# Kernel tuning notes

Hardware: AMD Instinct MI355X
Metric: run time of the kernel (lower is better)

## Reference

```python
import jax, jax.numpy as jnp
import numpy as np

B, IN, H, T = 64, 16, 512, 1024


def setup_inputs() -> dict:
    key = jax.random.key(0)
    ks = jax.random.split(key, 14)
    s = 0.05  # small init scale for numerically stable recurrence
    inp = {
        "x": jax.random.normal(ks[0], (B, IN), dtype=jnp.float32),
        "w_in": jax.random.normal(ks[1], (H, IN), dtype=jnp.float32) * s,
        "b_in": jax.random.normal(ks[2], (H,), dtype=jnp.float32) * s,
        "w_ih0": jax.random.normal(ks[3], (4 * H, H), dtype=jnp.float32) * s,
        "w_hh0": jax.random.normal(ks[4], (4 * H, H), dtype=jnp.float32) * s,
        "b_ih0": jax.random.normal(ks[5], (4 * H,), dtype=jnp.float32) * s,
        "b_hh0": jax.random.normal(ks[6], (4 * H,), dtype=jnp.float32) * s,
        "w_ih1": jax.random.normal(ks[7], (4 * H, H), dtype=jnp.float32) * s,
        "w_hh1": jax.random.normal(ks[8], (4 * H, H), dtype=jnp.float32) * s,
        "b_ih1": jax.random.normal(ks[9], (4 * H,), dtype=jnp.float32) * s,
        "b_hh1": jax.random.normal(ks[10], (4 * H,), dtype=jnp.float32) * s,
        "w_out": jax.random.normal(ks[11], (1, H), dtype=jnp.float32) * s,
        "b_out": jax.random.normal(ks[12], (1,), dtype=jnp.float32) * s,
        "seq_len": T,
    }
    return inp


def _lstm_layer(x_seq, w_ih, w_hh, b_ih, b_hh):
    # x_seq: [T, B, H] time-major. PyTorch gate order: i, f, g, o.
    # Precompute input-to-hidden projection for all steps at once.
    xg = jnp.einsum('tbh,gh->tbg', x_seq, w_ih) + b_ih  # [T, B, 4H]
    Bn = x_seq.shape[1]
    Hn = w_hh.shape[1]

    def step(carry, xg_t):
        h, c = carry
        g = xg_t + h @ w_hh.T + b_hh  # [B, 4H]
        i, f, gg, o = jnp.split(g, 4, axis=-1)
        c = jax.nn.sigmoid(f) * c + jax.nn.sigmoid(i) * jnp.tanh(gg)
        h = jax.nn.sigmoid(o) * jnp.tanh(c)
        return (h, c), h

    init = (jnp.zeros((Bn, Hn), x_seq.dtype), jnp.zeros((Bn, Hn), x_seq.dtype))
    _, hs = jax.lax.scan(step, init, xg)
    return hs  # [T, B, H]


def reference(x, w_in, b_in, w_ih0, w_hh0, b_ih0, b_hh0,
              w_ih1, w_hh1, b_ih1, b_hh1, w_out, b_out, seq_len):
    # fc_in then broadcast the identical input across all timesteps
    h_in = x @ w_in.T + b_in                      # [B, H]
    x_seq = jnp.broadcast_to(h_in[None], (seq_len, h_in.shape[0], h_in.shape[1]))
    h = _lstm_layer(x_seq, w_ih0, w_hh0, b_ih0, b_hh0)
    h = _lstm_layer(h, w_ih1, w_hh1, b_ih1, b_hh1)
    out = h @ w_out.T + b_out                     # [T, B, 1]
    return jnp.transpose(out, (1, 0, 2))          # [B, T, 1] (batch_first)
```

## Files before the change

kernel.cpp:

```cpp
#include <hip/hip_runtime.h>
#include <stdint.h>


#define TSEQ 1024
#define HDIM 512
#define BATCH 64
#define RING 8

typedef __attribute__((ext_vector_type(8))) short bf16x8;
typedef __attribute__((ext_vector_type(4))) float f32x4;
typedef __attribute__((ext_vector_type(4))) unsigned int u32x4;

__device__ __forceinline__ unsigned short f2bf(float f) {
  union { float f; unsigned u; } v; v.f = f;
  unsigned r = v.u + 0x7FFFu + ((v.u >> 16) & 1u);
  return (unsigned short)(r >> 16);
}
__device__ __forceinline__ float bf2f(unsigned short s) {
  union { unsigned u; float f; } v; v.u = ((unsigned)s) << 16; return v.f;
}
__device__ __forceinline__ float sigm(float x) { return 1.0f / (1.0f + __expf(-x)); }
__device__ __forceinline__ float tanh_(float x) { return 1.0f - 2.0f / (__expf(2.0f * x) + 1.0f); }

__device__ __forceinline__ void flag_add(int* p) {
  __hip_atomic_fetch_add(p, 1, __ATOMIC_RELAXED, __HIP_MEMORY_SCOPE_AGENT);
}
__device__ __forceinline__ void flag_wait(int* p, int target) {
  while (__hip_atomic_load(p, __ATOMIC_RELAXED, __HIP_MEMORY_SCOPE_AGENT) < target)
    __builtin_amdgcn_s_sleep(1);
}

__device__ __forceinline__ void stage64k(char* lds, const unsigned short* src, int tid) {
  u32x4 r0, r1, r2, r3, r4, r5, r6, r7;
  const char* a = (const char*)src + (size_t)tid * 16;
  asm volatile(
      "global_load_dwordx4 %0, %8, off sc1\n\t"
      "global_load_dwordx4 %1, %9, off sc1\n\t"
      "global_load_dwordx4 %2, %10, off sc1\n\t"
      "global_load_dwordx4 %3, %11, off sc1\n\t"
      "global_load_dwordx4 %4, %12, off sc1\n\t"
      "global_load_dwordx4 %5, %13, off sc1\n\t"
      "global_load_dwordx4 %6, %14, off sc1\n\t"
      "global_load_dwordx4 %7, %15, off sc1\n\t"
      "s_waitcnt vmcnt(0)"
      : "=&v"(r0), "=&v"(r1), "=&v"(r2), "=&v"(r3),
        "=&v"(r4), "=&v"(r5), "=&v"(r6), "=&v"(r7)
      : "v"(a), "v"(a + 8192), "v"(a + 16384), "v"(a + 24576),
        "v"(a + 32768), "v"(a + 40960), "v"(a + 49152), "v"(a + 57344)
      : "memory");
  u32x4 vv[8] = {r0, r1, r2, r3, r4, r5, r6, r7};
  #pragma unroll
  for (int i = 0; i < 8; ++i) {
    int q = tid + i * 512;
    int row = q >> 6, kb = (q & 63) << 4;
    *(u32x4*)(lds + row * 1024 + (kb ^ ((row & 7) << 4))) = vv[i];
  }
}
__device__ __forceinline__ void zero64k(char* lds, int tid) {
  u32x4 z = {0u, 0u, 0u, 0u};
  #pragma unroll
  for (int i = 0; i < 8; ++i) {
    int q = tid + i * 512;
    int row = q >> 6, kb = (q & 63) << 4;
    *(u32x4*)(lds + row * 1024 + (kb ^ ((row & 7) << 4))) = z;
  }
}

__global__ void k_fc_in(const float* __restrict__ x, const float* __restrict__ w_in,
                        const float* __restrict__ b_in, float* __restrict__ h_in) {
  int b = blockIdx.x;
  int j = threadIdx.x;
  float acc = b_in[j];
  #pragma unroll
  for (int i = 0; i < 16; ++i) acc += x[b * 16 + i] * w_in[j * 16 + i];
  h_in[b * HDIM + j] = acc;
}

__global__ __launch_bounds__(512, 1)
void k_xg0(const float* __restrict__ h_in, const float* __restrict__ w_ih0,
           const float* __restrict__ b_ih0, const float* __restrict__ b_hh0,
           float* __restrict__ xg0) {
  __shared__ float hbuf[64 * 516];
  __shared__ float wbuf[8 * 520];
  int r0 = blockIdx.x * 8;
  int tid = threadIdx.x;
  for (int i = 0; i < 64; ++i) {
    int c = tid + i * 512;
    hbuf[(c >> 9) * 516 + (c & 511)] = h_in[c];
  }
  for (int i = 0; i < 8; ++i) {
    int c = tid + i * 512;
    wbuf[(c >> 9) * 520 + (c & 511)] = w_ih0[(size_t)r0 * HDIM + c];
  }
  __syncthreads();
  int b = tid >> 3, rl = tid & 7;
  float acc = 0.f;
  for (int k = 0; k < 512; ++k) acc += hbuf[b * 516 + k] * wbuf[rl * 520 + k];
  int r = r0 + rl;
  xg0[(size_t)b * 2048 + r] = acc + b_ih0[r] + b_hh0[r];
}

__global__ __launch_bounds__(512, 1)
void lstm_persist(const float* __restrict__ w_hh0,
                  const float* __restrict__ w_ih1,
                  const float* __restrict__ w_hh1,
                  const float* __restrict__ b_ih1,
                  const float* __restrict__ b_hh1,
                  const float* __restrict__ w_out,
                  const float* __restrict__ b_out,
                  const float* __restrict__ xg0,
                  unsigned short* __restrict__ h0_ring,
                  unsigned short* __restrict__ h1_ring,
                  int* __restrict__ flags,
                  float* __restrict__ out) {
  __shared__ __align__(16) unsigned short hA[BATCH * HDIM];
  __shared__ __align__(16) unsigned short hBt[BATCH * HDIM];
  __shared__ float gbuf[BATCH * 68];
  char* hAc = (char*)hA;
  char* hBc = (char*)hBt;

  const int tid = threadIdx.x;
  const int layer = blockIdx.x & 1;
  const int p = blockIdx.x >> 1;
  const int u0 = p * 16;

  const int wave = tid >> 6, lane = tid & 63;
  const int nt = wave & 3;
  const int mh = wave >> 2;
  const int ln15 = lane & 15, lg = lane >> 4;

  const int n_local = nt * 16 + ln15;
  const int grow = (n_local & 3) * HDIM + u0 + (n_local >> 2);

  int* h0_ready = flags;
  int* h0_done  = flags + TSEQ;
  int* h1_ready = flags + 2 * TSEQ;
  int* h1_done  = flags + 3 * TSEQ;

  bf16x8 wh[16];
  bf16x8 wi[16];
  {
    const float* Wh = (layer == 0 ? w_hh0 : w_hh1) + (size_t)grow * HDIM;
    #pragma unroll
    for (int kt = 0; kt < 16; ++kt) {
      const float* s = Wh + kt * 32 + lg * 8;
      bf16x8 r;
      #pragma unroll
      for (int e = 0; e < 8; ++e) r[e] = (short)f2bf(s[e]);
      wh[kt] = r;
    }
  }
  if (layer == 1) {
    const float* Wi = w_ih1 + (size_t)grow * HDIM;
    #pragma unroll
    for (int kt = 0; kt < 16; ++kt) {
      const float* s = Wi + kt * 32 + lg * 8;
      bf16x8 r;
      #pragma unroll
      for (int e = 0; e < 8; ++e) r[e] = (short)f2bf(s[e]);
      wi[kt] = r;
    }
  }

  f32x4 init0, init1;
  if (layer == 0) {
    #pragma unroll
    for (int r = 0; r < 4; ++r) {
      init0[r] = xg0[(size_t)(mh * 32 + lg * 4 + r) * 2048 + grow];
      init1[r] = xg0[(size_t)(mh * 32 + 16 + lg * 4 + r) * 2048 + grow];
    }
  } else {
    float bv = b_ih1[grow] + b_hh1[grow];
    #pragma unroll
    for (int r = 0; r < 4; ++r) { init0[r] = bv; init1[r] = bv; }
  }

  float c0 = 0.f, c1 = 0.f;
  const int pb = tid >> 3;
  const int pu = (tid << 1) & 15;

  const int r0 = mh * 32 + ln15, r1 = r0 + 16;
  const int x0 = (r0 & 7) << 4, x1 = (r1 & 7) << 4;

  if (layer == 0) {
    for (int t = 0; t < TSEQ; ++t) {
      if (t > 0) {
        if (tid == 0) flag_wait(&h0_ready[t - 1], 32);
        __syncthreads();
        stage64k(hAc, h0_ring + (size_t)((t - 1) & (RING - 1)) * (BATCH * HDIM), tid);
        __syncthreads();
        if (tid == 0) flag_add(&h0_done[t - 1]);
      } else {
        zero64k(hAc, tid);
        __syncthreads();
      }
      f32x4 a0 = init0, a1 = init1;
      #pragma unroll
      for (int kt = 0; kt < 16; ++kt) {
        const int kb = kt * 64 + lg * 16;
        bf16x8 ha0 = *(const bf16x8*)(hAc + r0 * 1024 + (kb ^ x0));
        bf16x8 ha1 = *(const bf16x8*)(hAc + r1 * 1024 + (kb ^ x1));
        a0 = __builtin_amdgcn_mfma_f32_16x16x32_bf16(ha0, wh[kt], a0, 0, 0, 0);
        a1 = __builtin_amdgcn_mfma_f32_16x16x32_bf16(ha1, wh[kt], a1, 0, 0, 0);
      }
      #pragma unroll
      for (int r = 0; r < 4; ++r) {
        gbuf[(mh * 32 + lg * 4 + r) * 68 + n_local] = a0[r];
        gbuf[(mh * 32 + 16 + lg * 4 + r) * 68 + n_local] = a1[r];
      }
      if (t >= RING && tid == 0) flag_wait(&h0_done[t - RING], 64);
      __syncthreads();
      {
        f32x4 gA = *(const f32x4*)&gbuf[pb * 68 + pu * 4];
        f32x4 gB = *(const f32x4*)&gbuf[pb * 68 + pu * 4 + 4];
        float i0 = sigm(gA[0]), f0 = sigm(gA[1]), z0 = tanh_(gA[2]), o0 = sigm(gA[3]);
        float i1 = sigm(gB[0]), f1 = sigm(gB[1]), z1 = tanh_(gB[2]), o1 = sigm(gB[3]);
        c0 = f0 * c0 + i0 * z0;
        c1 = f1 * c1 + i1 * z1;
        float hv0 = o0 * tanh_(c0), hv1 = o1 * tanh_(c1);
        unsigned pk = (unsigned)f2bf(hv0) | ((unsigned)f2bf(hv1) << 16);
        unsigned short* slot = h0_ring + (size_t)(t & (RING - 1)) * (BATCH * HDIM);
        __hip_atomic_store((unsigned*)(slot + pb * HDIM + u0 + pu), pk,
                           __ATOMIC_RELAXED, __HIP_MEMORY_SCOPE_AGENT);
      }
      __syncthreads();
      if (tid == 0) flag_add(&h0_ready[t]);
    }
  } else {
    for (int t = 0; t < TSEQ; ++t) {
      if (tid == 0) {
        flag_wait(&h0_ready[t], 32);
        if (t > 0) flag_wait(&h1_ready[t - 1], 32);
      }
      __syncthreads();
      stage64k(hAc, h0_ring + (size_t)(t & (RING - 1)) * (BATCH * HDIM), tid);
      if (t > 0)
        stage64k(hBc, h1_ring + (size_t)((t - 1) & (RING - 1)) * (BATCH * HDIM), tid);
      else
        zero64k(hBc, tid);
      __syncthreads();
      if (tid == 0) {
        flag_add(&h0_done[t]);
        if (t > 0) flag_add(&h1_done[t - 1]);
      }

      if (t > 0 && tid < 16) {
        const int b = 2 * p + (tid >> 3), seg = tid & 7;
        const int xb = (b & 7) << 4;
        float acc = 0.f;
        #pragma unroll
        for (int i = 0; i < 8; ++i) {
          const int kb = seg * 128 + i * 16;
          bf16x8 hv = *(const bf16x8*)(hBc + b * 1024 + (kb ^ xb));
          const float* wo = w_out + (kb >> 1);
          #pragma unroll
          for (int e = 0; e < 8; ++e) acc += bf2f((unsigned short)hv[e]) * wo[e];
        }
        acc += __shfl_down(acc, 4, 8);
        acc += __shfl_down(acc, 2, 8);
        acc += __shfl_down(acc, 1, 8);
        if (seg == 0) out[b * TSEQ + (t - 1)] = acc + b_out[0];
      }

      f32x4 a0 = init0, a1 = init1;
      #pragma unroll
      for (int kt = 0; kt < 16; ++kt) {
        const int kb = kt * 64 + lg * 16;
        bf16x8 ia0 = *(const bf16x8*)(hAc + r0 * 1024 + (kb ^ x0));
        bf16x8 ia1 = *(const bf16x8*)(hAc + r1 * 1024 + (kb ^ x1));
        bf16x8 ha0 = *(const bf16x8*)(hBc + r0 * 1024 + (kb ^ x0));
        bf16x8 ha1 = *(const bf16x8*)(hBc + r1 * 1024 + (kb ^ x1));
        a0 = __builtin_amdgcn_mfma_f32_16x16x32_bf16(ia0, wi[kt], a0, 0, 0, 0);
        a1 = __builtin_amdgcn_mfma_f32_16x16x32_bf16(ia1, wi[kt], a1, 0, 0, 0);
        a0 = __builtin_amdgcn_mfma_f32_16x16x32_bf16(ha0, wh[kt], a0, 0, 0, 0);
        a1 = __builtin_amdgcn_mfma_f32_16x16x32_bf16(ha1, wh[kt], a1, 0, 0, 0);
      }
      #pragma unroll
      for (int r = 0; r < 4; ++r) {
        gbuf[(mh * 32 + lg * 4 + r) * 68 + n_local] = a0[r];
        gbuf[(mh * 32 + 16 + lg * 4 + r) * 68 + n_local] = a1[r];
      }
      if (t >= RING && tid == 0) flag_wait(&h1_done[t - RING], 32);
      __syncthreads();
      {
        f32x4 gA = *(const f32x4*)&gbuf[pb * 68 + pu * 4];
        f32x4 gB = *(const f32x4*)&gbuf[pb * 68 + pu * 4 + 4];
        float i0 = sigm(gA[0]), f0 = sigm(gA[1]), z0 = tanh_(gA[2]), o0 = sigm(gA[3]);
        float i1 = sigm(gB[0]), f1 = sigm(gB[1]), z1 = tanh_(gB[2]), o1 = sigm(gB[3]);
        c0 = f0 * c0 + i0 * z0;
        c1 = f1 * c1 + i1 * z1;
        float hv0 = o0 * tanh_(c0), hv1 = o1 * tanh_(c1);
        unsigned pk = (unsigned)f2bf(hv0) | ((unsigned)f2bf(hv1) << 16);
        unsigned short* slot = h1_ring + (size_t)(t & (RING - 1)) * (BATCH * HDIM);
        __hip_atomic_store((unsigned*)(slot + pb * HDIM + u0 + pu), pk,
                           __ATOMIC_RELAXED, __HIP_MEMORY_SCOPE_AGENT);
      }
      __syncthreads();
      if (tid == 0) flag_add(&h1_ready[t]);
    }
    if (tid == 0) flag_wait(&h1_ready[TSEQ - 1], 32);
    __syncthreads();
    stage64k(hBc, h1_ring + (size_t)((TSEQ - 1) & (RING - 1)) * (BATCH * HDIM), tid);
    __syncthreads();
    if (tid < 16) {
      const int b = 2 * p + (tid >> 3), seg = tid & 7;
      const int xb = (b & 7) << 4;
      float acc = 0.f;
      #pragma unroll
      for (int i = 0; i < 8; ++i) {
        const int kb = seg * 128 + i * 16;
        bf16x8 hv = *(const bf16x8*)(hBc + b * 1024 + (kb ^ xb));
        const float* wo = w_out + (kb >> 1);
        #pragma unroll
        for (int e = 0; e < 8; ++e) acc += bf2f((unsigned short)hv[e]) * wo[e];
      }
      acc += __shfl_down(acc, 4, 8);
      acc += __shfl_down(acc, 2, 8);
      acc += __shfl_down(acc, 1, 8);
      if (seg == 0) out[b * TSEQ + (TSEQ - 1)] = acc + b_out[0];
    }
  }
}

extern "C" void kernel_launch(void* const* d_in, const int* in_sizes, int n_in,
                              void* d_out, int out_size, void* d_ws, size_t ws_size,
                              hipStream_t stream) {
  (void)in_sizes; (void)n_in; (void)out_size; (void)ws_size;
  const float* x     = (const float*)d_in[0];
  const float* w_in  = (const float*)d_in[1];
  const float* b_in  = (const float*)d_in[2];
  const float* w_ih0 = (const float*)d_in[3];
  const float* w_hh0 = (const float*)d_in[4];
  const float* b_ih0 = (const float*)d_in[5];
  const float* b_hh0 = (const float*)d_in[6];
  const float* w_ih1 = (const float*)d_in[7];
  const float* w_hh1 = (const float*)d_in[8];
  const float* b_ih1 = (const float*)d_in[9];
  const float* b_hh1 = (const float*)d_in[10];
  const float* w_out = (const float*)d_in[11];
  const float* b_out = (const float*)d_in[12];

  char* ws = (char*)d_ws;
  unsigned short* h0_ring = (unsigned short*)(ws + 0);
  unsigned short* h1_ring = (unsigned short*)(ws + 524288);
  float* xg0  = (float*)(ws + 1048576);
  float* h_in = (float*)(ws + 1572864);
  int*   flags = (int*)(ws + 1703936);

  hipMemsetAsync(flags, 0, 4 * TSEQ * sizeof(int), stream);
  k_fc_in<<<64, 512, 0, stream>>>(x, w_in, b_in, h_in);
  k_xg0<<<256, 512, 0, stream>>>(h_in, w_ih0, b_ih0, b_hh0, xg0);
  lstm_persist<<<64, 512, 0, stream>>>(w_hh0, w_ih1, w_hh1, b_ih1, b_hh1,
                                       w_out, b_out, xg0, h0_ring, h1_ring,
                                       flags, (float*)d_out);
}
```

Measured before the change: 5.963 ms.

## Replace shared ready counters with per-producer sequence flags and packed publish

```diff
diff --git a/kernel.cpp b/kernel.cpp
--- a/kernel.cpp
+++ b/kernel.cpp
@@ -10,6 +10,7 @@
 typedef __attribute__((ext_vector_type(8))) short bf16x8;
 typedef __attribute__((ext_vector_type(4))) float f32x4;
 typedef __attribute__((ext_vector_type(4))) unsigned int u32x4;
+typedef unsigned long long u64;
 
 __device__ __forceinline__ unsigned short f2bf(float f) {
   union { float f; unsigned u; } v; v.f = f;
@@ -22,12 +23,24 @@
 __device__ __forceinline__ float sigm(float x) { return 1.0f / (1.0f + __expf(-x)); }
 __device__ __forceinline__ float tanh_(float x) { return 1.0f - 2.0f / (__expf(2.0f * x) + 1.0f); }
 
+__device__ __forceinline__ int g_ld32(const int* p) {
+  return __hip_atomic_load(p, __ATOMIC_RELAXED, __HIP_MEMORY_SCOPE_AGENT);
+}
+__device__ __forceinline__ void g_st32(int* p, int v) {
+  __hip_atomic_store(p, v, __ATOMIC_RELAXED, __HIP_MEMORY_SCOPE_AGENT);
+}
+__device__ __forceinline__ void g_st64(u64* p, u64 v) {
+  __hip_atomic_store(p, v, __ATOMIC_RELAXED, __HIP_MEMORY_SCOPE_AGENT);
+}
 __device__ __forceinline__ void flag_add(int* p) {
   __hip_atomic_fetch_add(p, 1, __ATOMIC_RELAXED, __HIP_MEMORY_SCOPE_AGENT);
 }
 __device__ __forceinline__ void flag_wait(int* p, int target) {
-  while (__hip_atomic_load(p, __ATOMIC_RELAXED, __HIP_MEMORY_SCOPE_AGENT) < target)
-    __builtin_amdgcn_s_sleep(1);
+  while (g_ld32(p) < target) __builtin_amdgcn_s_sleep(1);
+}
+__device__ __forceinline__ void poll_seq(const int* f, int tgt, int lane) {
+  const int* a = f + (lane & 31) * 4;
+  while (!__all(g_ld32(a) >= tgt)) __builtin_amdgcn_s_sleep(1);
 }
 
 __device__ __forceinline__ void stage64k(char* lds, const unsigned short* src, int tid) {
@@ -52,18 +65,26 @@
   #pragma unroll
   for (int i = 0; i < 8; ++i) {
     int q = tid + i * 512;
-    int row = q >> 6, kb = (q & 63) << 4;
-    *(u32x4*)(lds + row * 1024 + (kb ^ ((row & 7) << 4))) = vv[i];
+    int b = (q >> 1) & 63;
+    int col = (((q >> 7) << 5) | ((q & 1) << 4)) ^ ((b & 7) << 4);
+    *(u32x4*)(lds + b * 1024 + col) = vv[i];
   }
 }
 __device__ __forceinline__ void zero64k(char* lds, int tid) {
   u32x4 z = {0u, 0u, 0u, 0u};
   #pragma unroll
-  for (int i = 0; i < 8; ++i) {
-    int q = tid + i * 512;
-    int row = q >> 6, kb = (q & 63) << 4;
-    *(u32x4*)(lds + row * 1024 + (kb ^ ((row & 7) << 4))) = z;
-  }
+  for (int i = 0; i < 8; ++i)
+    *(u32x4*)(lds + (size_t)(tid + i * 512) * 16) = z;
+}
+
+__device__ __forceinline__ void publish2k(char* slotbase, int p, const unsigned short* hpk,
+                                          int lane, int* flagword, int val) {
+  const u64* s = (const u64*)(hpk + lane * 16);
+  u64 v0 = s[0], v1 = s[1], v2 = s[2], v3 = s[3];
+  u64* d = (u64*)(slotbase + p * 2048 + lane * 32);
+  g_st64(d + 0, v0); g_st64(d + 1, v1); g_st64(d + 2, v2); g_st64(d + 3, v3);
+  asm volatile("s_waitcnt vmcnt(0)" ::: "memory");
+  if (lane == 0) g_st32(flagword, val);
 }
 
 __global__ void k_fc_in(const float* __restrict__ x, const float* __restrict__ w_in,
@@ -109,13 +130,15 @@
                   const float* __restrict__ w_out,
                   const float* __restrict__ b_out,
                   const float* __restrict__ xg0,
-                  unsigned short* __restrict__ h0_ring,
-                  unsigned short* __restrict__ h1_ring,
+                  unsigned short* __restrict__ ring0,
+                  unsigned short* __restrict__ ring1,
                   int* __restrict__ flags,
                   float* __restrict__ out) {
   __shared__ __align__(16) unsigned short hA[BATCH * HDIM];
   __shared__ __align__(16) unsigned short hBt[BATCH * HDIM];
   __shared__ float gbuf[BATCH * 68];
+  __shared__ __align__(16) unsigned short hpk[BATCH * 16];
+  __shared__ float wout_s[HDIM];
   char* hAc = (char*)hA;
   char* hBc = (char*)hBt;
 
@@ -132,10 +155,13 @@
   const int n_local = nt * 16 + ln15;
   const int grow = (n_local & 3) * HDIM + u0 + (n_local >> 2);
 
-  int* h0_ready = flags;
-  int* h0_done  = flags + TSEQ;
-  int* h1_ready = flags + 2 * TSEQ;
-  int* h1_done  = flags + 3 * TSEQ;
+  int* f0 = flags;
+  int* f1 = flags + 128;
+  int* h0_done = flags + 256;
+  int* h1_done = flags + 256 + TSEQ;
+
+  wout_s[tid] = w_out[tid];
+  const float bout = b_out[0];
 
   bf16x8 wh[16];
   bf16x8 wi[16];
@@ -182,18 +208,19 @@
   const int r0 = mh * 32 + ln15, r1 = r0 + 16;
   const int x0 = (r0 & 7) << 4, x1 = (r1 & 7) << 4;
 
+  const int ob = tid >> 2, oseg = tid & 3;
+  const int oxs = (ob & 7) << 4;
+
   if (layer == 0) {
     for (int t = 0; t < TSEQ; ++t) {
-      if (t > 0) {
-        if (tid == 0) flag_wait(&h0_ready[t - 1], 32);
-        __syncthreads();
-        stage64k(hAc, h0_ring + (size_t)((t - 1) & (RING - 1)) * (BATCH * HDIM), tid);
-        __syncthreads();
-        if (tid == 0) flag_add(&h0_done[t - 1]);
-      } else {
-        zero64k(hAc, tid);
-        __syncthreads();
-      }
+      if (wave == 0) { if (t > 0) poll_seq(f0, t, lane); }
+      else if (wave == 1 && lane == 0 && t >= RING) flag_wait(&h0_done[t - RING], 64);
+      __syncthreads();
+      if (t > 0) stage64k(hAc, ring0 + (size_t)((t - 1) & (RING - 1)) * (BATCH * HDIM), tid);
+      else       zero64k(hAc, tid);
+      __syncthreads();
+      if (tid == 0 && t > 0) flag_add(&h0_done[t - 1]);
+
       f32x4 a0 = init0, a1 = init1;
       #pragma unroll
       for (int kt = 0; kt < 16; ++kt) {
@@ -208,58 +235,50 @@
         gbuf[(mh * 32 + lg * 4 + r) * 68 + n_local] = a0[r];
         gbuf[(mh * 32 + 16 + lg * 4 + r) * 68 + n_local] = a1[r];
       }
-      if (t >= RING && tid == 0) flag_wait(&h0_done[t - RING], 64);
       __syncthreads();
       {
         f32x4 gA = *(const f32x4*)&gbuf[pb * 68 + pu * 4];
         f32x4 gB = *(const f32x4*)&gbuf[pb * 68 + pu * 4 + 4];
-        float i0 = sigm(gA[0]), f0 = sigm(gA[1]), z0 = tanh_(gA[2]), o0 = sigm(gA[3]);
-        float i1 = sigm(gB[0]), f1 = sigm(gB[1]), z1 = tanh_(gB[2]), o1 = sigm(gB[3]);
-        c0 = f0 * c0 + i0 * z0;
-        c1 = f1 * c1 + i1 * z1;
-        float hv0 = o0 * tanh_(c0), hv1 = o1 * tanh_(c1);
-        unsigned pk = (unsigned)f2bf(hv0) | ((unsigned)f2bf(hv1) << 16);
-        unsigned short* slot = h0_ring + (size_t)(t & (RING - 1)) * (BATCH * HDIM);
-        __hip_atomic_store((unsigned*)(slot + pb * HDIM + u0 + pu), pk,
-                           __ATOMIC_RELAXED, __HIP_MEMORY_SCOPE_AGENT);
-      }
-      __syncthreads();
-      if (tid == 0) flag_add(&h0_ready[t]);
+        float i0 = sigm(gA[0]), f0v = sigm(gA[1]), z0 = tanh_(gA[2]), o0 = sigm(gA[3]);
+        float i1 = sigm(gB[0]), f1v = sigm(gB[1]), z1 = tanh_(gB[2]), o1 = sigm(gB[3]);
+        c0 = f0v * c0 + i0 * z0;
+        c1 = f1v * c1 + i1 * z1;
+        unsigned pk = (unsigned)f2bf(o0 * tanh_(c0)) | ((unsigned)f2bf(o1 * tanh_(c1)) << 16);
+        *(unsigned*)&hpk[pb * 16 + pu] = pk;
+      }
+      __syncthreads();
+      if (wave == 0)
+        publish2k((char*)(ring0 + (size_t)(t & (RING - 1)) * (BATCH * HDIM)),
+                  p, hpk, lane, &f0[p * 4], t + 1);
     }
   } else {
     for (int t = 0; t < TSEQ; ++t) {
-      if (tid == 0) {
-        flag_wait(&h0_ready[t], 32);
-        if (t > 0) flag_wait(&h1_ready[t - 1], 32);
-      }
-      __syncthreads();
-      stage64k(hAc, h0_ring + (size_t)(t & (RING - 1)) * (BATCH * HDIM), tid);
-      if (t > 0)
-        stage64k(hBc, h1_ring + (size_t)((t - 1) & (RING - 1)) * (BATCH * HDIM), tid);
-      else
-        zero64k(hBc, tid);
+      if (wave == 0) poll_seq(f0, t + 1, lane);
+      else if (wave == 1) { if (t > 0) poll_seq(f1, t, lane); }
+      else if (wave == 2 && lane == 0 && t >= RING) flag_wait(&h1_done[t - RING], 32);
+      __syncthreads();
+      stage64k(hAc, ring0 + (size_t)(t & (RING - 1)) * (BATCH * HDIM), tid);
+      if (t > 0) stage64k(hBc, ring1 + (size_t)((t - 1) & (RING - 1)) * (BATCH * HDIM), tid);
+      else       zero64k(hBc, tid);
       __syncthreads();
       if (tid == 0) {
         flag_add(&h0_done[t]);
         if (t > 0) flag_add(&h1_done[t - 1]);
       }
 
-      if (t > 0 && tid < 16) {
-        const int b = 2 * p + (tid >> 3), seg = tid & 7;
-        const int xb = (b & 7) << 4;
-        float acc = 0.f;
+      if (t > 0 && tid < 256) {
+        float od = 0.f;
         #pragma unroll
-        for (int i = 0; i < 8; ++i) {
-          const int kb = seg * 128 + i * 16;
-          bf16x8 hv = *(const bf16x8*)(hBc + b * 1024 + (kb ^ xb));
-          const float* wo = w_out + (kb >> 1);
+        for (int j = 0; j < 16; ++j) {
+          const int c = (j * 4 + oseg) * 16;
+          bf16x8 hv = *(const bf16x8*)(hBc + ob * 1024 + (c ^ oxs));
+          const float* wo = &wout_s[c >> 1];
           #pragma unroll
-          for (int e = 0; e < 8; ++e) acc += bf2f((unsigned short)hv[e]) * wo[e];
+          for (int e = 0; e < 8; ++e) od += bf2f((unsigned short)hv[e]) * wo[e];
         }
-        acc += __shfl_down(acc, 4, 8);
-        acc += __shfl_down(acc, 2, 8);
-        acc += __shfl_down(acc, 1, 8);
-        if (seg == 0) out[b * TSEQ + (t - 1)] = acc + b_out[0];
+        od += __shfl_xor(od, 1);
+        od += __shfl_xor(od, 2);
+        if (oseg == 0) out[ob * TSEQ + (t - 1)] = od + bout;
       }
 
       f32x4 a0 = init0, a1 = init1;
@@ -280,44 +299,39 @@
         gbuf[(mh * 32 + lg * 4 + r) * 68 + n_local] = a0[r];
         gbuf[(mh * 32 + 16 + lg * 4 + r) * 68 + n_local] = a1[r];
       }
-      if (t >= RING && tid == 0) flag_wait(&h1_done[t - RING], 32);
       __syncthreads();
       {
         f32x4 gA = *(const f32x4*)&gbuf[pb * 68 + pu * 4];
         f32x4 gB = *(const f32x4*)&gbuf[pb * 68 + pu * 4 + 4];
-        float i0 = sigm(gA[0]), f0 = sigm(gA[1]), z0 = tanh_(gA[2]), o0 = sigm(gA[3]);
-        float i1 = sigm(gB[0]), f1 = sigm(gB[1]), z1 = tanh_(gB[2]), o1 = sigm(gB[3]);
-        c0 = f0 * c0 + i0 * z0;
-        c1 = f1 * c1 + i1 * z1;
-        float hv0 = o0 * tanh_(c0), hv1 = o1 * tanh_(c1);
-        unsigned pk = (unsigned)f2bf(hv0) | ((unsigned)f2bf(hv1) << 16);
-        unsigned short* slot = h1_ring + (size_t)(t & (RING - 1)) * (BATCH * HDIM);
-        __hip_atomic_store((unsigned*)(slot + pb * HDIM + u0 + pu), pk,
-                           __ATOMIC_RELAXED, __HIP_MEMORY_SCOPE_AGENT);
-      }
-      __syncthreads();
-      if (tid == 0) flag_add(&h1_ready[t]);
-    }
-    if (tid == 0) flag_wait(&h1_ready[TSEQ - 1], 32);
+        float i0 = sigm(gA[0]), f0v = sigm(gA[1]), z0 = tanh_(gA[2]), o0 = sigm(gA[3]);
+        float i1 = sigm(gB[0]), f1v = sigm(gB[1]), z1 = tanh_(gB[2]), o1 = sigm(gB[3]);
+        c0 = f0v * c0 + i0 * z0;
+        c1 = f1v * c1 + i1 * z1;
+        unsigned pk = (unsigned)f2bf(o0 * tanh_(c0)) | ((unsigned)f2bf(o1 * tanh_(c1)) << 16);
+        *(unsigned*)&hpk[pb * 16 + pu] = pk;
+      }
+      __syncthreads();
+      if (wave == 0)
+        publish2k((char*)(ring1 + (size_t)(t & (RING - 1)) * (BATCH * HDIM)),
+                  p, hpk, lane, &f1[p * 4], t + 1);
+    }
+    if (wave == 0) poll_seq(f1, TSEQ, lane);
     __syncthreads();
-    stage64k(hBc, h1_ring + (size_t)((TSEQ - 1) & (RING - 1)) * (BATCH * HDIM), tid);
+    stage64k(hBc, ring1 + (size_t)((TSEQ - 1) & (RING - 1)) * (BATCH * HDIM), tid);
     __syncthreads();
-    if (tid < 16) {
-      const int b = 2 * p + (tid >> 3), seg = tid & 7;
-      const int xb = (b & 7) << 4;
-      float acc = 0.f;
-      #pragma unroll
-      for (int i = 0; i < 8; ++i) {
-        const int kb = seg * 128 + i * 16;
-        bf16x8 hv = *(const bf16x8*)(hBc + b * 1024 + (kb ^ xb));
-        const float* wo = w_out + (kb >> 1);
+    if (tid < 256) {
+      float od = 0.f;
+      #pragma unroll
+      for (int j = 0; j < 16; ++j) {
+        const int c = (j * 4 + oseg) * 16;
+        bf16x8 hv = *(const bf16x8*)(hBc + ob * 1024 + (c ^ oxs));
+        const float* wo = &wout_s[c >> 1];
         #pragma unroll
-        for (int e = 0; e < 8; ++e) acc += bf2f((unsigned short)hv[e]) * wo[e];
-      }
-      acc += __shfl_down(acc, 4, 8);
-      acc += __shfl_down(acc, 2, 8);
-      acc += __shfl_down(acc, 1, 8);
-      if (seg == 0) out[b * TSEQ + (TSEQ - 1)] = acc + b_out[0];
+        for (int e = 0; e < 8; ++e) od += bf2f((unsigned short)hv[e]) * wo[e];
+      }
+      od += __shfl_xor(od, 1);
+      od += __shfl_xor(od, 2);
+      if (oseg == 0) out[ob * TSEQ + (TSEQ - 1)] = od + bout;
     }
   }
 }
@@ -341,16 +355,16 @@
   const float* b_out = (const float*)d_in[12];
 
   char* ws = (char*)d_ws;
-  unsigned short* h0_ring = (unsigned short*)(ws + 0);
-  unsigned short* h1_ring = (unsigned short*)(ws + 524288);
+  unsigned short* ring0 = (unsigned short*)(ws + 0);
+  unsigned short* ring1 = (unsigned short*)(ws + 524288);
   float* xg0  = (float*)(ws + 1048576);
   float* h_in = (float*)(ws + 1572864);
   int*   flags = (int*)(ws + 1703936);
 
-  hipMemsetAsync(flags, 0, 4 * TSEQ * sizeof(int), stream);
+  hipMemsetAsync(flags, 0, 16384, stream);
   k_fc_in<<<64, 512, 0, stream>>>(x, w_in, b_in, h_in);
   k_xg0<<<256, 512, 0, stream>>>(h_in, w_ih0, b_ih0, b_hh0, xg0);
   lstm_persist<<<64, 512, 0, stream>>>(w_hh0, w_ih1, w_hh1, b_ih1, b_hh1,
-                                       w_out, b_out, xg0, h0_ring, h1_ring,
+                                       w_out, b_out, xg0, ring0, ring1,
                                        flags, (float*)d_out);
 }
```

Result: slower. 7.418 ms (+24.4%).

## Replace per-step atomic counter flags with per-block sequence flags polled by a wave

Applied to the files above, without the earlier changes.

```diff
diff --git a/kernel.cpp b/kernel.cpp
--- a/kernel.cpp
+++ b/kernel.cpp
@@ -22,12 +22,27 @@
 __device__ __forceinline__ float sigm(float x) { return 1.0f / (1.0f + __expf(-x)); }
 __device__ __forceinline__ float tanh_(float x) { return 1.0f - 2.0f / (__expf(2.0f * x) + 1.0f); }
 
+__device__ __forceinline__ int g_ld32(const int* p) {
+  return __hip_atomic_load(p, __ATOMIC_RELAXED, __HIP_MEMORY_SCOPE_AGENT);
+}
+__device__ __forceinline__ void g_st32(int* p, int v) {
+  __hip_atomic_store(p, v, __ATOMIC_RELAXED, __HIP_MEMORY_SCOPE_AGENT);
+}
 __device__ __forceinline__ void flag_add(int* p) {
   __hip_atomic_fetch_add(p, 1, __ATOMIC_RELAXED, __HIP_MEMORY_SCOPE_AGENT);
 }
 __device__ __forceinline__ void flag_wait(int* p, int target) {
-  while (__hip_atomic_load(p, __ATOMIC_RELAXED, __HIP_MEMORY_SCOPE_AGENT) < target)
-    __builtin_amdgcn_s_sleep(1);
+  while (g_ld32(p) < target) __builtin_amdgcn_s_sleep(1);
+}
+__device__ __forceinline__ void poll_seq(const int* f, int tgt, int lane) {
+  const int* a = f + (lane & 31) * 4;
+  while (!__all(g_ld32(a) >= tgt)) __builtin_amdgcn_s_sleep(1);
+}
+__device__ __forceinline__ void poll_seq2(const int* fa, int ta,
+                                          const int* fb, int tb, int lane) {
+  const int* a = (lane < 32) ? (fa + lane * 4) : (fb + (lane - 32) * 4);
+  const int tgt = (lane < 32) ? ta : tb;
+  while (!__all(g_ld32(a) >= tgt)) __builtin_amdgcn_s_sleep(1);
 }
 
 __device__ __forceinline__ void stage64k(char* lds, const unsigned short* src, int tid) {
@@ -132,10 +147,10 @@
   const int n_local = nt * 16 + ln15;
   const int grow = (n_local & 3) * HDIM + u0 + (n_local >> 2);
 
-  int* h0_ready = flags;
-  int* h0_done  = flags + TSEQ;
-  int* h1_ready = flags + 2 * TSEQ;
-  int* h1_done  = flags + 3 * TSEQ;
+  int* f0seq = flags;
+  int* f1seq = flags + 128;
+  int* h0_done = flags + 256;
+  int* h1_done = flags + 256 + TSEQ;
 
   bf16x8 wh[16];
   bf16x8 wi[16];
@@ -184,9 +199,9 @@
 
   if (layer == 0) {
     for (int t = 0; t < TSEQ; ++t) {
+      if (t > 0 && wave == 0) poll_seq(f0seq, t, lane);
+      __syncthreads();
       if (t > 0) {
-        if (tid == 0) flag_wait(&h0_ready[t - 1], 32);
-        __syncthreads();
         stage64k(hAc, h0_ring + (size_t)((t - 1) & (RING - 1)) * (BATCH * HDIM), tid);
         __syncthreads();
         if (tid == 0) flag_add(&h0_done[t - 1]);
@@ -224,14 +239,11 @@
                            __ATOMIC_RELAXED, __HIP_MEMORY_SCOPE_AGENT);
       }
       __syncthreads();
-      if (tid == 0) flag_add(&h0_ready[t]);
+      if (tid == 0) g_st32(&f0seq[p * 4], t + 1);
     }
   } else {
     for (int t = 0; t < TSEQ; ++t) {
-      if (tid == 0) {
-        flag_wait(&h0_ready[t], 32);
-        if (t > 0) flag_wait(&h1_ready[t - 1], 32);
-      }
+      if (wave == 0) poll_seq2(f0seq, t + 1, f1seq, t, lane);
       __syncthreads();
       stage64k(hAc, h0_ring + (size_t)(t & (RING - 1)) * (BATCH * HDIM), tid);
       if (t > 0)
@@ -296,9 +308,9 @@
                            __ATOMIC_RELAXED, __HIP_MEMORY_SCOPE_AGENT);
       }
       __syncthreads();
-      if (tid == 0) flag_add(&h1_ready[t]);
-    }
-    if (tid == 0) flag_wait(&h1_ready[TSEQ - 1], 32);
+      if (tid == 0) g_st32(&f1seq[p * 4], t + 1);
+    }
+    if (wave == 0) poll_seq(f1seq, TSEQ, lane);
     __syncthreads();
     stage64k(hBc, h1_ring + (size_t)((TSEQ - 1) & (RING - 1)) * (BATCH * HDIM), tid);
     __syncthreads();
@@ -347,7 +359,7 @@
   float* h_in = (float*)(ws + 1572864);
   int*   flags = (int*)(ws + 1703936);
 
-  hipMemsetAsync(flags, 0, 4 * TSEQ * sizeof(int), stream);
+  hipMemsetAsync(flags, 0, 16384, stream);
   k_fc_in<<<64, 512, 0, stream>>>(x, w_in, b_in, h_in);
   k_xg0<<<256, 512, 0, stream>>>(h_in, w_ih0, b_ih0, b_hh0, xg0);
   lstm_persist<<<64, 512, 0, stream>>>(w_hh0, w_ih1, w_hh1, b_ih1, b_hh1,
```

Measured after the change: 6.333 ms. +6.2%, slower.

## Replace ready-flag handshakes with per-word timestep tags in hidden-state ring

Applied to the files above, without the earlier changes.

```diff
diff --git a/kernel.cpp b/kernel.cpp
--- a/kernel.cpp
+++ b/kernel.cpp
@@ -29,41 +29,63 @@
   while (__hip_atomic_load(p, __ATOMIC_RELAXED, __HIP_MEMORY_SCOPE_AGENT) < target)
     __builtin_amdgcn_s_sleep(1);
 }
-
-__device__ __forceinline__ void stage64k(char* lds, const unsigned short* src, int tid) {
-  u32x4 r0, r1, r2, r3, r4, r5, r6, r7;
-  const char* a = (const char*)src + (size_t)tid * 16;
-  asm volatile(
-      "global_load_dwordx4 %0, %8, off sc1\n\t"
-      "global_load_dwordx4 %1, %9, off sc1\n\t"
-      "global_load_dwordx4 %2, %10, off sc1\n\t"
-      "global_load_dwordx4 %3, %11, off sc1\n\t"
-      "global_load_dwordx4 %4, %12, off sc1\n\t"
-      "global_load_dwordx4 %5, %13, off sc1\n\t"
-      "global_load_dwordx4 %6, %14, off sc1\n\t"
-      "global_load_dwordx4 %7, %15, off sc1\n\t"
-      "s_waitcnt vmcnt(0)"
-      : "=&v"(r0), "=&v"(r1), "=&v"(r2), "=&v"(r3),
-        "=&v"(r4), "=&v"(r5), "=&v"(r6), "=&v"(r7)
-      : "v"(a), "v"(a + 8192), "v"(a + 16384), "v"(a + 24576),
-        "v"(a + 32768), "v"(a + 40960), "v"(a + 49152), "v"(a + 57344)
-      : "memory");
-  u32x4 vv[8] = {r0, r1, r2, r3, r4, r5, r6, r7};
+__device__ __forceinline__ void g_st32u(unsigned* p, unsigned v) {
+  __hip_atomic_store(p, v, __ATOMIC_RELAXED, __HIP_MEMORY_SCOPE_AGENT);
+}
+
+__device__ __forceinline__ void stage_tag(char* lds, const unsigned* src32,
+                                          int tid, int tag) {
   #pragma unroll
-  for (int i = 0; i < 8; ++i) {
-    int q = tid + i * 512;
-    int row = q >> 6, kb = (q & 63) << 4;
-    *(u32x4*)(lds + row * 1024 + (kb ^ ((row & 7) << 4))) = vv[i];
+  for (int half = 0; half < 2; ++half) {
+    u32x4 r0, r1, r2, r3, r4, r5, r6, r7;
+    const char* a = (const char*)src32 + (size_t)tid * 32 + (size_t)half * 65536;
+    while (true) {
+      asm volatile(
+          "global_load_dwordx4 %0, %8, off sc1\n\t"
+          "global_load_dwordx4 %1, %9, off sc1\n\t"
+          "global_load_dwordx4 %2, %10, off sc1\n\t"
+          "global_load_dwordx4 %3, %11, off sc1\n\t"
+          "global_load_dwordx4 %4, %12, off sc1\n\t"
+          "global_load_dwordx4 %5, %13, off sc1\n\t"
+          "global_load_dwordx4 %6, %14, off sc1\n\t"
+          "global_load_dwordx4 %7, %15, off sc1\n\t"
+          "s_waitcnt vmcnt(0)"
+          : "=&v"(r0), "=&v"(r1), "=&v"(r2), "=&v"(r3),
+            "=&v"(r4), "=&v"(r5), "=&v"(r6), "=&v"(r7)
+          : "v"(a), "v"(a + 16), "v"(a + 16384), "v"(a + 16400),
+            "v"(a + 32768), "v"(a + 32784), "v"(a + 49152), "v"(a + 49168)
+          : "memory");
+      bool ok = true;
+      #pragma unroll
+      for (int j = 0; j < 4; ++j) {
+        ok &= ((r0[j] & 0xffffu) == (unsigned)tag) & ((r1[j] & 0xffffu) == (unsigned)tag);
+        ok &= ((r2[j] & 0xffffu) == (unsigned)tag) & ((r3[j] & 0xffffu) == (unsigned)tag);
+        ok &= ((r4[j] & 0xffffu) == (unsigned)tag) & ((r5[j] & 0xffffu) == (unsigned)tag);
+        ok &= ((r6[j] & 0xffffu) == (unsigned)tag) & ((r7[j] & 0xffffu) == (unsigned)tag);
+      }
+      if (__all(ok)) break;
+      __builtin_amdgcn_s_sleep(1);
+    }
+    u32x4 lo[4] = {r0, r2, r4, r6};
+    u32x4 hi[4] = {r1, r3, r5, r7};
+    #pragma unroll
+    for (int j = 0; j < 4; ++j) {
+      int q = tid + (4 * half + j) * 512;
+      int row = q >> 6, kb = (q & 63) << 4;
+      u32x4 outq;
+      outq[0] = (lo[j][1] & 0xffff0000u) | (lo[j][0] >> 16);
+      outq[1] = (lo[j][3] & 0xffff0000u) | (lo[j][2] >> 16);
+      outq[2] = (hi[j][1] & 0xffff0000u) | (hi[j][0] >> 16);
+      outq[3] = (hi[j][3] & 0xffff0000u) | (hi[j][2] >> 16);
+      *(u32x4*)(lds + row * 1024 + (kb ^ ((row & 7) << 4))) = outq;
+    }
   }
 }
 __device__ __forceinline__ void zero64k(char* lds, int tid) {
   u32x4 z = {0u, 0u, 0u, 0u};
   #pragma unroll
-  for (int i = 0; i < 8; ++i) {
-    int q = tid + i * 512;
-    int row = q >> 6, kb = (q & 63) << 4;
-    *(u32x4*)(lds + row * 1024 + (kb ^ ((row & 7) << 4))) = z;
-  }
+  for (int i = 0; i < 8; ++i)
+    *(u32x4*)(lds + (size_t)(tid + i * 512) * 16) = z;
 }
 
 __global__ void k_fc_in(const float* __restrict__ x, const float* __restrict__ w_in,
@@ -109,8 +131,8 @@
                   const float* __restrict__ w_out,
                   const float* __restrict__ b_out,
                   const float* __restrict__ xg0,
-                  unsigned short* __restrict__ h0_ring,
-                  unsigned short* __restrict__ h1_ring,
+                  unsigned* __restrict__ ring0,
+                  unsigned* __restrict__ ring1,
                   int* __restrict__ flags,
                   float* __restrict__ out) {
   __shared__ __align__(16) unsigned short hA[BATCH * HDIM];
@@ -132,10 +154,8 @@
   const int n_local = nt * 16 + ln15;
   const int grow = (n_local & 3) * HDIM + u0 + (n_local >> 2);
 
-  int* h0_ready = flags;
-  int* h0_done  = flags + TSEQ;
-  int* h1_ready = flags + 2 * TSEQ;
-  int* h1_done  = flags + 3 * TSEQ;
+  int* h0_done = flags;
+  int* h1_done = flags + TSEQ;
 
   bf16x8 wh[16];
   bf16x8 wi[16];
@@ -182,18 +202,15 @@
   const int r0 = mh * 32 + ln15, r1 = r0 + 16;
   const int x0 = (r0 & 7) << 4, x1 = (r1 & 7) << 4;
 
+  const size_t SL32 = (size_t)BATCH * HDIM;
+
   if (layer == 0) {
     for (int t = 0; t < TSEQ; ++t) {
-      if (t > 0) {
-        if (tid == 0) flag_wait(&h0_ready[t - 1], 32);
-        __syncthreads();
-        stage64k(hAc, h0_ring + (size_t)((t - 1) & (RING - 1)) * (BATCH * HDIM), tid);
-        __syncthreads();
-        if (tid == 0) flag_add(&h0_done[t - 1]);
-      } else {
-        zero64k(hAc, tid);
-        __syncthreads();
-      }
+      if (t > 0) stage_tag(hAc, ring0 + (size_t)((t - 1) & (RING - 1)) * SL32, tid, t - 1);
+      else       zero64k(hAc, tid);
+      __syncthreads();
+      if (tid == 0 && t > 0) flag_add(&h0_done[t - 1]);
+
       f32x4 a0 = init0, a1 = init1;
       #pragma unroll
       for (int kt = 0; kt < 16; ++kt) {
@@ -217,27 +234,18 @@
         float i1 = sigm(gB[0]), f1 = sigm(gB[1]), z1 = tanh_(gB[2]), o1 = sigm(gB[3]);
         c0 = f0 * c0 + i0 * z0;
         c1 = f1 * c1 + i1 * z1;
-        float hv0 = o0 * tanh_(c0), hv1 = o1 * tanh_(c1);
-        unsigned pk = (unsigned)f2bf(hv0) | ((unsigned)f2bf(hv1) << 16);
-        unsigned short* slot = h0_ring + (size_t)(t & (RING - 1)) * (BATCH * HDIM);
-        __hip_atomic_store((unsigned*)(slot + pb * HDIM + u0 + pu), pk,
-                           __ATOMIC_RELAXED, __HIP_MEMORY_SCOPE_AGENT);
-      }
-      __syncthreads();
-      if (tid == 0) flag_add(&h0_ready[t]);
+        unsigned w0 = ((unsigned)f2bf(o0 * tanh_(c0)) << 16) | (unsigned)t;
+        unsigned w1 = ((unsigned)f2bf(o1 * tanh_(c1)) << 16) | (unsigned)t;
+        unsigned* slot = ring0 + (size_t)(t & (RING - 1)) * SL32 + pb * HDIM + u0 + pu;
+        g_st32u(slot, w0);
+        g_st32u(slot + 1, w1);
+      }
     }
   } else {
     for (int t = 0; t < TSEQ; ++t) {
-      if (tid == 0) {
-        flag_wait(&h0_ready[t], 32);
-        if (t > 0) flag_wait(&h1_ready[t - 1], 32);
-      }
-      __syncthreads();
-      stage64k(hAc, h0_ring + (size_t)(t & (RING - 1)) * (BATCH * HDIM), tid);
-      if (t > 0)
-        stage64k(hBc, h1_ring + (size_t)((t - 1) & (RING - 1)) * (BATCH * HDIM), tid);
-      else
-        zero64k(hBc, tid);
+      stage_tag(hAc, ring0 + (size_t)(t & (RING - 1)) * SL32, tid, t);
+      if (t > 0) stage_tag(hBc, ring1 + (size_t)((t - 1) & (RING - 1)) * SL32, tid, t - 1);
+      else       zero64k(hBc, tid);
       __syncthreads();
       if (tid == 0) {
         flag_add(&h0_done[t]);
@@ -289,18 +297,14 @@
         float i1 = sigm(gB[0]), f1 = sigm(gB[1]), z1 = tanh_(gB[2]), o1 = sigm(gB[3]);
         c0 = f0 * c0 + i0 * z0;
         c1 = f1 * c1 + i1 * z1;
-        float hv0 = o0 * tanh_(c0), hv1 = o1 * tanh_(c1);
-        unsigned pk = (unsigned)f2bf(hv0) | ((unsigned)f2bf(hv1) << 16);
-        unsigned short* slot = h1_ring + (size_t)(t & (RING - 1)) * (BATCH * HDIM);
-        __hip_atomic_store((unsigned*)(slot + pb * HDIM + u0 + pu), pk,
-                           __ATOMIC_RELAXED, __HIP_MEMORY_SCOPE_AGENT);
-      }
-      __syncthreads();
-      if (tid == 0) flag_add(&h1_ready[t]);
-    }
-    if (tid == 0) flag_wait(&h1_ready[TSEQ - 1], 32);
-    __syncthreads();
-    stage64k(hBc, h1_ring + (size_t)((TSEQ - 1) & (RING - 1)) * (BATCH * HDIM), tid);
+        unsigned w0 = ((unsigned)f2bf(o0 * tanh_(c0)) << 16) | (unsigned)t;
+        unsigned w1 = ((unsigned)f2bf(o1 * tanh_(c1)) << 16) | (unsigned)t;
+        unsigned* slot = ring1 + (size_t)(t & (RING - 1)) * SL32 + pb * HDIM + u0 + pu;
+        g_st32u(slot, w0);
+        g_st32u(slot + 1, w1);
+      }
+    }
+    stage_tag(hBc, ring1 + (size_t)((TSEQ - 1) & (RING - 1)) * SL32, tid, TSEQ - 1);
     __syncthreads();
     if (tid < 16) {
       const int b = 2 * p + (tid >> 3), seg = tid & 7;
@@ -341,16 +345,17 @@
   const float* b_out = (const float*)d_in[12];
 
   char* ws = (char*)d_ws;
-  unsigned short* h0_ring = (unsigned short*)(ws + 0);
-  unsigned short* h1_ring = (unsigned short*)(ws + 524288);
-  float* xg0  = (float*)(ws + 1048576);
-  float* h_in = (float*)(ws + 1572864);
-  int*   flags = (int*)(ws + 1703936);
-
-  hipMemsetAsync(flags, 0, 4 * TSEQ * sizeof(int), stream);
+  unsigned* ring0 = (unsigned*)(ws + 0);
+  unsigned* ring1 = (unsigned*)(ws + 1048576);
+  float* xg0  = (float*)(ws + 2097152);
+  float* h_in = (float*)(ws + 2621440);
+  int*   flags = (int*)(ws + 2752512);
+
+  hipMemsetAsync(ring0, 0xFF, 2097152, stream);
+  hipMemsetAsync(flags, 0, 2 * TSEQ * sizeof(int), stream);
   k_fc_in<<<64, 512, 0, stream>>>(x, w_in, b_in, h_in);
   k_xg0<<<256, 512, 0, stream>>>(h_in, w_ih0, b_ih0, b_hh0, xg0);
   lstm_persist<<<64, 512, 0, stream>>>(w_hh0, w_ih1, w_hh1, b_ih1, b_hh1,
-                                       w_out, b_out, xg0, h0_ring, h1_ring,
+                                       w_out, b_out, xg0, ring0, ring1,
                                        flags, (float*)d_out);
 }
```

Result: slower. 7.823 ms (+31.2%).
